# Optimization experiments

Measured on AMD Instinct MI355X. Metric: run time of the kernel, lower is better.

The kernel has to match this reference:

```python
import jax, jax.numpy as jnp
import numpy as np

N, E, G = 20000, 320000, 256
FXD, FXT, OD = 78, 954, 128


def _lin(key, fan_in, fan_out, scale=0.05):
    return jax.random.normal(key, (fan_in, fan_out), dtype=jnp.float32) * scale


def setup_inputs() -> dict:
    key = jax.random.key(0)
    ks = jax.random.split(key, 24)
    inp = {
        "x1": jax.random.normal(ks[0], (N, FXD), dtype=jnp.float32),
        "edge_index1": jax.random.randint(ks[1], (2, E), 0, N, dtype=jnp.int32),
        "batch1": (jnp.arange(N, dtype=jnp.int32) * G) // N,  # sorted, every graph non-empty
        "x2": jax.random.normal(ks[2], (N, FXD), dtype=jnp.float32),
        "edge_index2": jax.random.randint(ks[3], (2, E), 0, N, dtype=jnp.int32),
        "batch2": (jnp.arange(N, dtype=jnp.int32) * G) // N,
        "cell": jax.random.normal(ks[4], (G, FXT), dtype=jnp.float32),
        # GCNConv weights (shared across the two drug branches, as in the module)
        "Wc1": _lin(ks[5], FXD, FXD), "bc1": jnp.zeros((FXD,), jnp.float32),
        "Wc2": _lin(ks[6], FXD, FXD * 2), "bc2": jnp.zeros((FXD * 2,), jnp.float32),
        "Wc3": _lin(ks[7], FXD * 2, FXD * 4), "bc3": jnp.zeros((FXD * 4,), jnp.float32),
        "Wg1": _lin(ks[8], FXD * 4, FXD * 2), "bg1": jnp.zeros((FXD * 2,), jnp.float32),
        "Wg2": _lin(ks[9], FXD * 2, OD), "bg2": jnp.zeros((OD,), jnp.float32),
        # cell reduction MLP 954 -> 2048 -> 512 -> 256
        "Wr1": _lin(ks[10], FXT, 2048), "br1": jnp.zeros((2048,), jnp.float32),
        "Wr2": _lin(ks[11], 2048, 512), "br2": jnp.zeros((512,), jnp.float32),
        "Wr3": _lin(ks[12], 512, OD * 2), "br3": jnp.zeros((OD * 2,), jnp.float32),
        # head MLP 512 -> 1024 -> 512 -> 128 -> 2
        "Wf1": _lin(ks[13], OD * 4, 1024), "bf1": jnp.zeros((1024,), jnp.float32),
        "Wf2": _lin(ks[14], 1024, 512), "bf2": jnp.zeros((512,), jnp.float32),
        "Wf3": _lin(ks[15], 512, 128), "bf3": jnp.zeros((128,), jnp.float32),
        "Wo": _lin(ks[16], 128, 2), "bo": jnp.zeros((2,), jnp.float32),
    }
    return inp


def gcn_conv(x, W, b, src, dst, n):
    """PyG GCNConv: h = D^{-1/2}(A+I)D^{-1/2} (x W) + b (self-loops added)."""
    h = x @ W
    loops = jnp.arange(n, dtype=src.dtype)
    s = jnp.concatenate([src, loops])
    d = jnp.concatenate([dst, loops])
    deg = jax.ops.segment_sum(jnp.ones_like(s, dtype=h.dtype), d, num_segments=n)
    dinv = jax.lax.rsqrt(deg)  # deg >= 1 due to self-loops
    norm = dinv[s] * dinv[d]  # [E+N]
    out = jax.ops.segment_sum(h[s] * norm[:, None], d, num_segments=n)
    return out + b


def drug_branch(x, ei, batch, Wc1, bc1, Wc2, bc2, Wc3, bc3, Wg1, bg1, Wg2, bg2):
    src, dst = ei[0], ei[1]
    n = x.shape[0]
    x = jax.nn.relu(gcn_conv(x, Wc1, bc1, src, dst, n))
    x = jax.nn.relu(gcn_conv(x, Wc2, bc2, src, dst, n))
    x = jax.nn.relu(gcn_conv(x, Wc3, bc3, src, dst, n))
    x = jax.ops.segment_max(x, batch, num_segments=G)  # global max pool -> [G, 312]
    x = jax.nn.relu(x @ Wg1 + bg1)
    x = x @ Wg2 + bg2  # dropout is identity in eval mode
    return x


def reference(x1, edge_index1, batch1, x2, edge_index2, batch2, cell,
              Wc1, bc1, Wc2, bc2, Wc3, bc3, Wg1, bg1, Wg2, bg2,
              Wr1, br1, Wr2, br2, Wr3, br3,
              Wf1, bf1, Wf2, bf2, Wf3, bf3, Wo, bo):
    g1 = drug_branch(x1, edge_index1, batch1, Wc1, bc1, Wc2, bc2, Wc3, bc3, Wg1, bg1, Wg2, bg2)
    g2 = drug_branch(x2, edge_index2, batch2, Wc1, bc1, Wc2, bc2, Wc3, bc3, Wg1, bg1, Wg2, bg2)
    # F.normalize(cell, p=2, dim=1)
    cv = cell / jnp.maximum(jnp.linalg.norm(cell, axis=1, keepdims=True), 1e-12)
    cv = jax.nn.relu(cv @ Wr1 + br1)
    cv = jax.nn.relu(cv @ Wr2 + br2)
    cv = jax.nn.relu(cv @ Wr3 + br3)
    xc = jnp.concatenate([g1, g2, cv], axis=1)  # [G, 512]
    xc = jax.nn.relu(xc @ Wf1 + bf1)
    xc = jax.nn.relu(xc @ Wf2 + bf2)
    xc = jax.nn.relu(xc @ Wf3 + bf3)
    return xc @ Wo + bo  # [G, 2]
```

## Files before the change

### kernel.cpp

```cpp
#include <hip/hip_runtime.h>

#define N_NODES 20000
#define N_EDGES 320000
#define N_GRAPH 256
#define ECHUNK 2048

__device__ __forceinline__ ushort f2b(float f) {
  unsigned u = __float_as_uint(f);
  u += 0x7FFFu + ((u >> 16) & 1u);
  return (ushort)(u >> 16);
}
__device__ __forceinline__ float b2f(ushort u) {
  return __uint_as_float(((unsigned)u) << 16);
}

typedef __attribute__((ext_vector_type(8))) short bf16x8;
typedef __attribute__((ext_vector_type(4))) float f32x4;

template <int POOL>
__launch_bounds__(256)
__global__ void gemm_mfma(const ushort* __restrict__ A, int lda,
                          const ushort* __restrict__ Bt, int ldbt,
                          void* __restrict__ Cv, int ldc, int zstride,
                          const float* __restrict__ bias,
                          int Nr, int Kpad, int M, int do_relu, int obf,
                          int kchunk, int swz,
                          const int* __restrict__ bA, const int* __restrict__ bB,
                          int nsplit, int gA, int gB, int gTot) {
  constexpr int BM = 128, BN = 64, BK = 32, LK = 40;
  __shared__ __align__(16) ushort Asl[BM][LK];
  __shared__ __align__(16) ushort Bsl[BN][LK];
  const int tid = threadIdx.x;
  int bx, by;
  if (swz) {
    const int Cc = (M + BN - 1) / BN;
    const int R = (Nr + BM - 1) / BM;
    const int RR = (R + 7) >> 3;
    const int xz = blockIdx.x & 7, g = blockIdx.x >> 3;
    const int q = g / Cc;
    by = xz * RR + q;
    bx = g - q * Cc;
    if (by >= R) return;
  } else {
    bx = blockIdx.x; by = blockIdx.y;
  }
  const int row0 = by * BM, col0 = bx * BN;

  const int lane = tid & 63, w = tid >> 6;
  const int a_r = tid >> 1, a_h = tid & 1;
  const int b_r = tid >> 2, b_o = (tid & 3) * 8;

  const int klo = blockIdx.z * kchunk;
  const int khi = min(klo + kchunk, Kpad);
  const int nst = (khi - klo) / BK;

  uint4 pa0, pa1, pb0;
  auto load_tile = [&](int k0) {
    if (row0 + a_r < Nr) {
      const uint4* p = (const uint4*)(A + (size_t)(row0 + a_r) * lda + k0 + a_h * 16);
      pa0 = p[0]; pa1 = p[1];
    } else {
      pa0 = make_uint4(0u, 0u, 0u, 0u); pa1 = pa0;
    }
    pb0 = *(const uint4*)(Bt + (size_t)(col0 + b_r) * ldbt + k0 + b_o);
  };
  auto commit = [&]() {
    *(uint4*)&Asl[a_r][a_h * 16] = pa0;
    *(uint4*)&Asl[a_r][a_h * 16 + 8] = pa1;
    *(uint4*)&Bsl[b_r][b_o] = pb0;
  };

  f32x4 acc[2][4] = {};
  const int mrow = w * 32;
  const int lm = lane & 15, lq = (lane >> 4) * 8;

  load_tile(klo);
  for (int t = 0; t < nst; ++t) {
    commit();
    __syncthreads();
    if (t + 1 < nst) load_tile(klo + (t + 1) * BK);
    bf16x8 af0 = *(const bf16x8*)&Asl[mrow + lm][lq];
    bf16x8 af1 = *(const bf16x8*)&Asl[mrow + 16 + lm][lq];
    bf16x8 bf0 = *(const bf16x8*)&Bsl[lm][lq];
    bf16x8 bf1 = *(const bf16x8*)&Bsl[16 + lm][lq];
    bf16x8 bf2 = *(const bf16x8*)&Bsl[32 + lm][lq];
    bf16x8 bf3 = *(const bf16x8*)&Bsl[48 + lm][lq];
    acc[0][0] = __builtin_amdgcn_mfma_f32_16x16x32_bf16(af0, bf0, acc[0][0], 0, 0, 0);
    acc[0][1] = __builtin_amdgcn_mfma_f32_16x16x32_bf16(af0, bf1, acc[0][1], 0, 0, 0);
    acc[0][2] = __builtin_amdgcn_mfma_f32_16x16x32_bf16(af0, bf2, acc[0][2], 0, 0, 0);
    acc[0][3] = __builtin_amdgcn_mfma_f32_16x16x32_bf16(af0, bf3, acc[0][3], 0, 0, 0);
    acc[1][0] = __builtin_amdgcn_mfma_f32_16x16x32_bf16(af1, bf0, acc[1][0], 0, 0, 0);
    acc[1][1] = __builtin_amdgcn_mfma_f32_16x16x32_bf16(af1, bf1, acc[1][1], 0, 0, 0);
    acc[1][2] = __builtin_amdgcn_mfma_f32_16x16x32_bf16(af1, bf2, acc[1][2], 0, 0, 0);
    acc[1][3] = __builtin_amdgcn_mfma_f32_16x16x32_bf16(af1, bf3, acc[1][3], 0, 0, 0);
    __syncthreads();
  }

  const int rquad = (lane >> 4) * 4;

  if constexpr (POOL) {
    __shared__ int Ps[4][64];
    Ps[tid >> 6][tid & 63] = 0;
    __syncthreads();
    const int g0 = (row0 < nsplit) ? gA + bA[row0] : gB + bB[row0 - nsplit];
    int gr8[2][4];
#pragma unroll
    for (int mt = 0; mt < 2; ++mt)
#pragma unroll
      for (int r = 0; r < 4; ++r) {
        const int rr = row0 + mrow + mt * 16 + rquad + r;
        gr8[mt][r] = (rr < Nr)
                         ? ((rr < nsplit) ? gA + bA[rr] : gB + bB[rr - nsplit])
                         : -1;
      }
#pragma unroll
    for (int mt = 0; mt < 2; ++mt)
#pragma unroll
      for (int nt = 0; nt < 4; ++nt) {
        const int cl = nt * 16 + lm;
        if (col0 + cl >= M) continue;
        const float bv = bias[col0 + cl];
#pragma unroll
        for (int r = 0; r < 4; ++r) {
          const int g = gr8[mt][r];
          if (g < 0) continue;
          const float v = fmaxf(acc[mt][nt][r] + bv, 0.f);
          atomicMax(&Ps[g - g0][cl], __float_as_int(v));
        }
      }
    __syncthreads();
    const int s = tid >> 6, c = tid & 63;
    const int g = g0 + s, cc = col0 + c;
    if (g < gTot && cc < M)
      atomicMax((int*)Cv + (size_t)g * ldc + cc, Ps[s][c]);
    return;
  }

  if (zstride) {
    float* Cz = (float*)Cv + (size_t)blockIdx.z * zstride;
#pragma unroll
    for (int mt = 0; mt < 2; ++mt)
#pragma unroll
      for (int nt = 0; nt < 4; ++nt) {
        const int cc = col0 + nt * 16 + lm;
        if (cc >= M) continue;
#pragma unroll
        for (int r = 0; r < 4; ++r) {
          const int rr = row0 + mrow + mt * 16 + rquad + r;
          if (rr < Nr) Cz[(size_t)rr * ldc + cc] = acc[mt][nt][r];
        }
      }
    return;
  }
#pragma unroll
  for (int mt = 0; mt < 2; ++mt) {
#pragma unroll
    for (int nt = 0; nt < 4; ++nt) {
      const int cc = col0 + nt * 16 + lm;
      if (cc >= M) continue;
      const float bv = bias ? bias[cc] : 0.f;
#pragma unroll
      for (int r = 0; r < 4; ++r) {
        const int rr = row0 + mrow + mt * 16 + rquad + r;
        if (rr >= Nr) continue;
        float v = acc[mt][nt][r] + bv;
        if (do_relu) v = fmaxf(v, 0.f);
        if (obf) ((ushort*)Cv)[(size_t)rr * ldc + cc] = f2b(v);
        else     ((float*)Cv)[(size_t)rr * ldc + cc] = v;
      }
    }
  }
}

struct GJob {
  const void* A; const ushort* Bt; void* C; const float* bias;
  int lda, a_f32, ldbt, ldc, Nr, Kpad, M, relu, obf, rsplit, cpad, rb, cb, blk0;
};

__launch_bounds__(256)
__global__ void gemm_grp(GJob j0, GJob j1, int njobs) {
  GJob j = (njobs > 1 && (int)blockIdx.x >= j1.blk0) ? j1 : j0;
  const int local = blockIdx.x - j.blk0;
  const int by = local / j.cb, bx = local - by * j.cb;
  const int row0 = by * 32, col0 = bx * 64;
  const int tid = threadIdx.x, lane = tid & 63, w = tid >> 6;

  __shared__ __align__(16) char smem[32768];
  ushort (*Asl)[32][40] = (ushort (*)[32][40])smem;
  ushort (*Bsl)[64][40] = (ushort (*)[64][40])(smem + 10240);
  float  (*Rs)[32][64]  = (float  (*)[32][64])smem;

  const int a_r = lane >> 1, a_h = lane & 1;
  const int lm = lane & 15, lq = (lane >> 4) * 8;
  const int nst = j.Kpad / 32;

  uint4 ra[4], rb[4];
  auto gload = [&](int t) {
    const int k0 = t * 32;
    const int ar = row0 + a_r;
    if (j.a_f32) {
      if (ar < j.Nr) {
        const uint4* p = (const uint4*)((const float*)j.A + (size_t)ar * j.lda + k0 + a_h * 16);
        ra[0] = p[0]; ra[1] = p[1]; ra[2] = p[2]; ra[3] = p[3];
      } else {
        ra[0] = make_uint4(0u, 0u, 0u, 0u); ra[1] = ra[0]; ra[2] = ra[0]; ra[3] = ra[0];
      }
    } else {
      if (ar < j.Nr) {
        const uint4* p = (const uint4*)((const ushort*)j.A + (size_t)ar * j.lda + k0 + a_h * 16);
        ra[0] = p[0]; ra[1] = p[1];
      } else {
        ra[0] = make_uint4(0u, 0u, 0u, 0u); ra[1] = ra[0];
      }
    }
    const uint4* q = (const uint4*)(j.Bt + (size_t)(col0 + lane) * j.ldbt + k0);
    rb[0] = q[0]; rb[1] = q[1]; rb[2] = q[2]; rb[3] = q[3];
  };
  auto commit = [&]() {
    if (j.a_f32) {
      ushort tmp[16];
      const float* f = (const float*)&ra[0];
#pragma unroll
      for (int q2 = 0; q2 < 16; ++q2) tmp[q2] = f2b(f[q2]);
      *(uint4*)&Asl[w][a_r][a_h * 16]     = *(uint4*)&tmp[0];
      *(uint4*)&Asl[w][a_r][a_h * 16 + 8] = *(uint4*)&tmp[8];
    } else {
      *(uint4*)&Asl[w][a_r][a_h * 16]     = ra[0];
      *(uint4*)&Asl[w][a_r][a_h * 16 + 8] = ra[1];
    }
    *(uint4*)&Bsl[w][lane][0]  = rb[0];
    *(uint4*)&Bsl[w][lane][8]  = rb[1];
    *(uint4*)&Bsl[w][lane][16] = rb[2];
    *(uint4*)&Bsl[w][lane][24] = rb[3];
  };

  f32x4 acc[2][4] = {};
  if (w < nst) {
    gload(w);
    for (int t = w; t < nst; t += 4) {
      commit();
      bf16x8 af0 = *(const bf16x8*)&Asl[w][lm][lq];
      bf16x8 af1 = *(const bf16x8*)&Asl[w][16 + lm][lq];
      bf16x8 bq0 = *(const bf16x8*)&Bsl[w][lm][lq];
      bf16x8 bq1 = *(const bf16x8*)&Bsl[w][16 + lm][lq];
      bf16x8 bq2 = *(const bf16x8*)&Bsl[w][32 + lm][lq];
      bf16x8 bq3 = *(const bf16x8*)&Bsl[w][48 + lm][lq];
      if (t + 4 < nst) gload(t + 4);
      acc[0][0] = __builtin_amdgcn_mfma_f32_16x16x32_bf16(af0, bq0, acc[0][0], 0, 0, 0);
      acc[0][1] = __builtin_amdgcn_mfma_f32_16x16x32_bf16(af0, bq1, acc[0][1], 0, 0, 0);
      acc[0][2] = __builtin_amdgcn_mfma_f32_16x16x32_bf16(af0, bq2, acc[0][2], 0, 0, 0);
      acc[0][3] = __builtin_amdgcn_mfma_f32_16x16x32_bf16(af0, bq3, acc[0][3], 0, 0, 0);
      acc[1][0] = __builtin_amdgcn_mfma_f32_16x16x32_bf16(af1, bq0, acc[1][0], 0, 0, 0);
      acc[1][1] = __builtin_amdgcn_mfma_f32_16x16x32_bf16(af1, bq1, acc[1][1], 0, 0, 0);
      acc[1][2] = __builtin_amdgcn_mfma_f32_16x16x32_bf16(af1, bq2, acc[1][2], 0, 0, 0);
      acc[1][3] = __builtin_amdgcn_mfma_f32_16x16x32_bf16(af1, bq3, acc[1][3], 0, 0, 0);
    }
  }

  __syncthreads();
  const int rquad = (lane >> 4) * 4;
#pragma unroll
  for (int mt = 0; mt < 2; ++mt)
#pragma unroll
    for (int nt = 0; nt < 4; ++nt)
#pragma unroll
      for (int r = 0; r < 4; ++r)
        Rs[w][mt * 16 + rquad + r][nt * 16 + lm] = acc[mt][nt][r];
  __syncthreads();

  const int rrow = tid >> 3, cs = (tid & 7) * 8;
  float v[8];
  {
    float4 x0 = *(const float4*)&Rs[0][rrow][cs];
    float4 x1 = *(const float4*)&Rs[0][rrow][cs + 4];
    v[0] = x0.x; v[1] = x0.y; v[2] = x0.z; v[3] = x0.w;
    v[4] = x1.x; v[5] = x1.y; v[6] = x1.z; v[7] = x1.w;
  }
#pragma unroll
  for (int ww = 1; ww < 4; ++ww) {
    float4 x0 = *(const float4*)&Rs[ww][rrow][cs];
    float4 x1 = *(const float4*)&Rs[ww][rrow][cs + 4];
    v[0] += x0.x; v[1] += x0.y; v[2] += x0.z; v[3] += x0.w;
    v[4] += x1.x; v[5] += x1.y; v[6] += x1.z; v[7] += x1.w;
  }
  const int rg = row0 + rrow;
  if (rg < j.Nr) {
    int rm = rg, rq = 0;
    if (j.rsplit) { rq = rg / j.rsplit; rm = rg - rq * j.rsplit; }
#pragma unroll
    for (int q = 0; q < 8; ++q) {
      const int cc = col0 + cs + q;
      if (cc >= j.cpad) break;
      float x = 0.f;
      if (cc < j.M) {
        x = v[q] + j.bias[cc];
        if (j.relu) x = fmaxf(x, 0.f);
      }
      const size_t di = (size_t)rm * j.ldc + (size_t)rq * j.M + cc;
      if (j.obf) ((ushort*)j.C)[di] = f2b(x);
      else       ((float*)j.C)[di] = x;
    }
  }
}

struct WJob { const float* W; ushort* T; int Mv, Kv, Mp, Kp, blk0; };
struct WArgs { WJob j[11]; int wblocks; const float* cell; ushort* cv; };

__launch_bounds__(256)
__global__ void prep_all(WArgs a) {
  __shared__ float red[256];
  const int bid = blockIdx.x, tid = threadIdx.x;
  if (bid < a.wblocks) {
    int ji = 0;
#pragma unroll
    for (int i = 1; i < 11; ++i)
      if (bid >= a.j[i].blk0) ji = i;
    WJob wj = a.j[ji];
    int el = (bid - wj.blk0) * 256 + tid;
    if (el < wj.Mp * wj.Kp) {
      int n = el / wj.Kp, k = el - n * wj.Kp;
      wj.T[el] = (n < wj.Mv && k < wj.Kv) ? f2b(wj.W[(size_t)k * wj.Mv + n]) : 0;
    }
    return;
  }
  const int g = bid - a.wblocks;
  const float* row = a.cell + (size_t)g * 954;
  float s = 0.f;
  for (int f = tid; f < 954; f += 256) { float vv = row[f]; s += vv * vv; }
  red[tid] = s;
  __syncthreads();
  for (int off2 = 128; off2 > 0; off2 >>= 1) {
    if (tid < off2) red[tid] += red[tid + off2];
    __syncthreads();
  }
  const float inv = 1.f / fmaxf(sqrtf(red[0]), 1e-12f);
  ushort* orow = a.cv + (size_t)g * 960;
  for (int f = tid; f < 954; f += 256) orow[f] = f2b(row[f] * inv);
  for (int f = 954 + tid; f < 960; f += 256) orow[f] = 0;
}

template<int BM, int BN, int TM, int TN>
__launch_bounds__(256)
__global__ void gemm_t(const float* __restrict__ A, int lda,
                       const float* __restrict__ B, int ldb,
                       float* __restrict__ C, int ldc, int zstride,
                       const float* __restrict__ bias,
                       int Nr, int K, int M, int do_relu, int kchunk) {
  constexpr int BK = 16;
  constexpr int LDA = BM + 4;
  __shared__ __align__(16) float As[BK][LDA];
  __shared__ __align__(16) float Bs[BK][BN];
  const int tid = threadIdx.x;
  const int row0 = blockIdx.y * BM, col0 = blockIdx.x * BN;
  constexpr int NX = BN / TN;
  const int tx = tid % NX, ty = tid / NX;
  float acc[TM][TN] = {};
  const int klo = blockIdx.z * kchunk;
  const int khi = min(klo + kchunk, K);

  constexpr int AIT = BM * BK / 4 / 256;
  constexpr int BIT = BK * BN / 4 / 256;
  float4 pa[AIT], pb[BIT];

  auto load_tile = [&](int k0) {
#pragma unroll
    for (int it = 0; it < AIT; ++it) {
      const int s = it * 256 + tid;
      const int row = s >> 2, kq = (s & 3) << 2;
      float4 av = make_float4(0.f, 0.f, 0.f, 0.f);
      const int gr = row0 + row, gk = k0 + kq;
      if (gr < Nr) {
        const float* Ap = A + (size_t)gr * lda + gk;
        if (gk + 3 < khi) { av.x = Ap[0]; av.y = Ap[1]; av.z = Ap[2]; av.w = Ap[3]; }
        else {
          if (gk     < khi) av.x = Ap[0];
          if (gk + 1 < khi) av.y = Ap[1];
          if (gk + 2 < khi) av.z = Ap[2];
        }
      }
      pa[it] = av;
    }
#pragma unroll
    for (int it = 0; it < BIT; ++it) {
      const int s = it * 256 + tid;
      const int kr = s / (BN / 4), c = (s % (BN / 4)) << 2;
      float4 bv = make_float4(0.f, 0.f, 0.f, 0.f);
      const int gk = k0 + kr, gc = col0 + c;
      if (gk < khi) {
        const float* Bp = B + (size_t)gk * ldb + gc;
        if (gc + 3 < M) { bv.x = Bp[0]; bv.y = Bp[1]; bv.z = Bp[2]; bv.w = Bp[3]; }
        else {
          if (gc     < M) bv.x = Bp[0];
          if (gc + 1 < M) bv.y = Bp[1];
          if (gc + 2 < M) bv.z = Bp[2];
        }
      }
      pb[it] = bv;
    }
  };

  load_tile(klo);
  for (int k0 = klo; k0 < khi; k0 += BK) {
#pragma unroll
    for (int it = 0; it < AIT; ++it) {
      const int s = it * 256 + tid;
      const int row = s >> 2, kq = (s & 3) << 2;
      As[kq    ][row] = pa[it].x;
      As[kq + 1][row] = pa[it].y;
      As[kq + 2][row] = pa[it].z;
      As[kq + 3][row] = pa[it].w;
    }
#pragma unroll
    for (int it = 0; it < BIT; ++it) {
      const int s = it * 256 + tid;
      const int kr = s / (BN / 4), c = (s % (BN / 4)) << 2;
      *(float4*)&Bs[kr][c] = pb[it];
    }
    __syncthreads();
    if (k0 + BK < khi) load_tile(k0 + BK);
#pragma unroll
    for (int kk = 0; kk < BK; ++kk) {
      float ar[TM], br[TN];
#pragma unroll
      for (int i = 0; i < TM; i += 4)
        *(float4*)&ar[i] = *(const float4*)&As[kk][ty * TM + i];
      if constexpr (TN == 8) {
        *(float4*)&br[0] = *(const float4*)&Bs[kk][tx * 4];
        *(float4*)&br[4] = *(const float4*)&Bs[kk][BN / 2 + tx * 4];
      } else {
        *(float4*)&br[0] = *(const float4*)&Bs[kk][tx * TN];
      }
#pragma unroll
      for (int i = 0; i < TM; ++i)
#pragma unroll
        for (int j = 0; j < TN; ++j)
          acc[i][j] += ar[i] * br[j];
    }
    __syncthreads();
  }

  float* Cz = C + (size_t)blockIdx.z * zstride;
#pragma unroll
  for (int i = 0; i < TM; ++i) {
    const int r = row0 + ty * TM + i;
    if (r >= Nr) continue;
    float* Crow = Cz + (size_t)r * ldc;
#pragma unroll
    for (int g = 0; g < TN / 4; ++g) {
      const int c = col0 + (TN == 8 ? g * (BN / 2) : 0) + tx * 4;
      if (c + 3 < M) {
        float4 v;
        v.x = acc[i][g * 4 + 0]; v.y = acc[i][g * 4 + 1];
        v.z = acc[i][g * 4 + 2]; v.w = acc[i][g * 4 + 3];
        if (bias) { v.x += bias[c]; v.y += bias[c + 1]; v.z += bias[c + 2]; v.w += bias[c + 3]; }
        if (do_relu) {
          v.x = fmaxf(v.x, 0.f); v.y = fmaxf(v.y, 0.f);
          v.z = fmaxf(v.z, 0.f); v.w = fmaxf(v.w, 0.f);
        }
        *(float4*)&Crow[c] = v;
      } else {
#pragma unroll
        for (int j = 0; j < 4; ++j) {
          if (c + j >= M) continue;
          float v = acc[i][g * 4 + j];
          if (bias) v += bias[c + j];
          if (do_relu) v = fmaxf(v, 0.f);
          Crow[c + j] = v;
        }
      }
    }
  }
}

__global__ void histp_kernel(const int* __restrict__ e1, const int* __restrict__ e2,
                             int* __restrict__ cnt, int E, int npass, int rng) {
  const int xcd = blockIdx.x & 7;
  const int lo = xcd * rng, hi = lo + rng;
  const int base = (blockIdx.x >> 3) * ECHUNK;
  const int TE = npass * E;
  for (int i = threadIdx.x; i < ECHUNK; i += 256) {
    int e = base + i;
    if (e >= TE) break;
    int d = (e < E) ? e1[E + e] : N_NODES + e2[e - E + E];
    if (d >= lo && d < hi) atomicAdd(&cnt[d], 1);
  }
}

__global__ void scat_cvt_kernel(const int* __restrict__ e1, const int* __restrict__ e2,
                                int* __restrict__ cursor, ushort* __restrict__ col_idx,
                                int E, int npass, int rng, int scat_blocks,
                                const float* __restrict__ xa, const float* __restrict__ xb,
                                int nsplit, ushort* __restrict__ dst, int total16) {
  if ((int)blockIdx.x < scat_blocks) {
    const int xcd = blockIdx.x & 7;
    const int lo = xcd * rng, hi = lo + rng;
    const int base = (blockIdx.x >> 3) * ECHUNK;
    const int TE = npass * E;
    for (int i = threadIdx.x; i < ECHUNK; i += 256) {
      int e = base + i;
      if (e >= TE) break;
      int d, s;
      if (e < E) { d = e1[E + e]; s = e1[e]; }
      else { int jj = e - E; d = N_NODES + e2[E + jj]; s = N_NODES + e2[jj]; }
      if (d >= lo && d < hi) {
        int p = atomicAdd(&cursor[d], 1);
        col_idx[p] = (ushort)s;
      }
    }
    return;
  }
  int gid = (blockIdx.x - scat_blocks) * 256 + threadIdx.x;
  if (gid >= total16) return;
  int n = gid / 20, v = gid - n * 20;
  const float* src = (n < nsplit) ? xa + (size_t)n * 78 : xb + (size_t)(n - nsplit) * 78;
  int f0 = v * 4;
  ushort4 o;
  o.x = (f0     < 78) ? f2b(src[f0])     : 0;
  o.y = (f0 + 1 < 78) ? f2b(src[f0 + 1]) : 0;
  o.z = (f0 + 2 < 78) ? f2b(src[f0 + 2]) : 0;
  o.w = (f0 + 3 < 78) ? f2b(src[f0 + 3]) : 0;
  ((ushort4*)(dst + (size_t)n * 80))[v] = o;
}

__launch_bounds__(1024)
__global__ void scan1_kernel(const int* __restrict__ cnt, int* __restrict__ row_ptr,
                             int* __restrict__ part, int n) {
  __shared__ int sh[1024];
  const int tid = threadIdx.x;
  const int i = blockIdx.x * 1024 + tid;
  const int v = (i < n) ? cnt[i] : 0;
  sh[tid] = v;
  __syncthreads();
#pragma unroll
  for (int off = 1; off < 1024; off <<= 1) {
    int t = (tid >= off) ? sh[tid - off] : 0;
    __syncthreads();
    sh[tid] += t;
    __syncthreads();
  }
  if (i < n) row_ptr[i] = sh[tid] - v;
  if (tid == 1023) part[blockIdx.x] = sh[tid];
}

__global__ void scan23_kernel(const int* __restrict__ cnt, int* __restrict__ row_ptr,
                              const int* __restrict__ part, int* __restrict__ cursor,
                              float* __restrict__ dinv, int n, int total,
                              const int* __restrict__ b1, const int* __restrict__ b2,
                              int* __restrict__ s1, int* __restrict__ s2) {
  __shared__ int base_sh;
  const int tid = threadIdx.x;
  if (tid == 0) {
    int blk = blockIdx.x >> 2;
    int s = 0;
    for (int b = 0; b < blk; ++b) s += part[b];
    base_sh = s;
  }
  __syncthreads();
  int i = blockIdx.x * 256 + tid;
  if (i >= n) return;
  int rp = row_ptr[i] + base_sh;
  row_ptr[i] = rp;
  cursor[i] = rp;
  dinv[i] = rsqrtf((float)(cnt[i] + 1));
  if (i == 0) row_ptr[n] = total;
  if (i < N_NODES) {
    if (i == 0) { s1[0] = 0; s1[N_GRAPH] = N_NODES; }
    else if (b1[i] != b1[i - 1]) s1[b1[i]] = i;
  } else {
    int j = i - N_NODES;
    if (j == 0) { s2[0] = N_NODES; s2[N_GRAPH] = 2 * N_NODES; }
    else if (b2[j] != b2[j - 1]) s2[b2[j]] = N_NODES + j;
  }
}

__global__ void aggb_flat(const ushort* __restrict__ h, const int* __restrict__ row_ptr,
                          const ushort* __restrict__ col_idx, const float* __restrict__ dinv,
                          ushort* __restrict__ out, int in_ld, int out_ld,
                          int V, int total) {
  int gid = blockIdx.x * blockDim.x + threadIdx.x;
  if (gid >= total) return;
  int n = gid / V, v = gid - n * V;
  const float din = dinv[n];
  const ushort4* hv = (const ushort4*)h;
  const int ivs = in_ld >> 2;
  float4 a;
  {
    ushort4 u = hv[(size_t)n * ivs + v];
    a.x = din * b2f(u.x); a.y = din * b2f(u.y);
    a.z = din * b2f(u.z); a.w = din * b2f(u.w);
  }
  const int beg = row_ptr[n], end = row_ptr[n + 1];
  int e = beg;
  for (; e + 3 < end; e += 4) {
    int s0 = col_idx[e], s1 = col_idx[e + 1], s2 = col_idx[e + 2], s3 = col_idx[e + 3];
    float d0 = dinv[s0], d1 = dinv[s1], d2 = dinv[s2], d3 = dinv[s3];
    ushort4 u0 = hv[(size_t)s0 * ivs + v], u1 = hv[(size_t)s1 * ivs + v];
    ushort4 u2 = hv[(size_t)s2 * ivs + v], u3 = hv[(size_t)s3 * ivs + v];
    a.x += d0 * b2f(u0.x) + d1 * b2f(u1.x) + d2 * b2f(u2.x) + d3 * b2f(u3.x);
    a.y += d0 * b2f(u0.y) + d1 * b2f(u1.y) + d2 * b2f(u2.y) + d3 * b2f(u3.y);
    a.z += d0 * b2f(u0.z) + d1 * b2f(u1.z) + d2 * b2f(u2.z) + d3 * b2f(u3.z);
    a.w += d0 * b2f(u0.w) + d1 * b2f(u1.w) + d2 * b2f(u2.w) + d3 * b2f(u3.w);
  }
  for (; e < end; ++e) {
    int s0 = col_idx[e];
    float d0 = dinv[s0];
    ushort4 u0 = hv[(size_t)s0 * ivs + v];
    a.x += d0 * b2f(u0.x); a.y += d0 * b2f(u0.y);
    a.z += d0 * b2f(u0.z); a.w += d0 * b2f(u0.w);
  }
  ushort4 o;
  o.x = f2b(din * a.x); o.y = f2b(din * a.y);
  o.z = f2b(din * a.z); o.w = f2b(din * a.w);
  ((ushort4*)(out + (size_t)n * out_ld))[v] = o;
}

extern "C" void kernel_launch(void* const* d_in, const int* in_sizes, int n_in,
                              void* d_out, int out_size, void* d_ws, size_t ws_size,
                              hipStream_t stream) {
  (void)in_sizes; (void)n_in; (void)out_size;
  const float* x1  = (const float*)d_in[0];
  const int*   ei1 = (const int*)d_in[1];
  const int*   bt1 = (const int*)d_in[2];
  const float* x2  = (const float*)d_in[3];
  const int*   ei2 = (const int*)d_in[4];
  const int*   bt2 = (const int*)d_in[5];
  const float* cell = (const float*)d_in[6];
  const float* Wc1 = (const float*)d_in[7];  const float* bc1 = (const float*)d_in[8];
  const float* Wc2 = (const float*)d_in[9];  const float* bc2 = (const float*)d_in[10];
  const float* Wc3 = (const float*)d_in[11]; const float* bc3 = (const float*)d_in[12];
  const float* Wg1 = (const float*)d_in[13]; const float* bg1 = (const float*)d_in[14];
  const float* Wg2 = (const float*)d_in[15]; const float* bg2 = (const float*)d_in[16];
  const float* Wr1 = (const float*)d_in[17]; const float* br1 = (const float*)d_in[18];
  const float* Wr2 = (const float*)d_in[19]; const float* br2 = (const float*)d_in[20];
  const float* Wr3 = (const float*)d_in[21]; const float* br3 = (const float*)d_in[22];
  const float* Wf1 = (const float*)d_in[23]; const float* bf1 = (const float*)d_in[24];
  const float* Wf2 = (const float*)d_in[25]; const float* bf2 = (const float*)d_in[26];
  const float* Wf3 = (const float*)d_in[27]; const float* bf3 = (const float*)d_in[28];
  const float* Wo  = (const float*)d_in[29]; const float* bo  = (const float*)d_in[30];
  float* out = (float*)d_out;

  const bool batched = ws_size >= (size_t)95 * 1024 * 1024;
  const int NPASS = batched ? 2 : 1;
  const int NN = NPASS * N_NODES;

  char* ws = (char*)d_ws;
  size_t off = 0;
  auto alloc_f = [&](size_t ne) {
    ne = (ne + 3) & ~(size_t)3;
    float* p = (float*)(ws + off); off += ne * 4; return p;
  };
  auto alloc_i = [&](size_t ne) {
    ne = (ne + 3) & ~(size_t)3;
    int* p = (int*)(ws + off); off += ne * 4; return p;
  };
  ushort* xb16w = (ushort*)alloc_f((size_t)NN * 80);
  ushort* ab16  = (ushort*)alloc_f((size_t)NN * 80);
  ushort* xb16s = (ushort*)alloc_f((size_t)NN * 40);
  float* dinv   = alloc_f(NN);
  int* cnt      = alloc_i(NN);
  float* pooled = alloc_f((size_t)512 * 320);
  ushort* cv16  = (ushort*)alloc_f((size_t)N_GRAPH * 480);
  ushort* wg1o  = (ushort*)alloc_f((size_t)512 * 80);
  ushort* wr1o  = (ushort*)alloc_f((size_t)256 * 1024);
  ushort* wr2o  = (ushort*)alloc_f((size_t)256 * 256);
  ushort* catbuf = (ushort*)alloc_f((size_t)256 * 256);
  ushort* wf1o  = (ushort*)alloc_f((size_t)256 * 512);
  ushort* wf2o  = (ushort*)alloc_f((size_t)256 * 256);
  float* wf3o   = alloc_f((size_t)256 * 128);
  ushort* wc1t  = (ushort*)alloc_f(128 * 96 / 2);
  ushort* wc2t  = (ushort*)alloc_f(192 * 96 / 2);
  ushort* wc3t  = (ushort*)alloc_f(320 * 160 / 2);
  ushort* wr1t  = (ushort*)alloc_f(2048 * 960 / 2);
  ushort* wr2t  = (ushort*)alloc_f(512 * 2048 / 2);
  ushort* wf1t  = (ushort*)alloc_f(1024 * 512 / 2);
  ushort* wg1t  = (ushort*)alloc_f(192 * 320 / 2);
  ushort* wg2t  = (ushort*)alloc_f(128 * 160 / 2);
  ushort* wr3t  = (ushort*)alloc_f(256 * 512 / 2);
  ushort* wf2t  = (ushort*)alloc_f(512 * 1024 / 2);
  ushort* wf3t  = (ushort*)alloc_f(128 * 512 / 2);
  int* row_ptr = alloc_i(NN + 4);
  int* cursor  = alloc_i(NN);
  ushort* col_idx = (ushort*)alloc_i(NPASS * N_EDGES / 2);
  int* part    = alloc_i(64);
  int* start1  = alloc_i(N_GRAPH + 4);
  int* start2  = alloc_i(N_GRAPH + 4);

  auto gemm_small = [&](const float* A, int lda, const float* B, int ldb, float* C, int ldc,
                        const float* bias, int Nr, int K, int M, int relu) {
    dim3 grid((M + 63) / 64, (Nr + 63) / 64, 1);
    gemm_t<64, 64, 4, 4><<<grid, 256, 0, stream>>>(A, lda, B, ldb, C, ldc, 0, bias,
                                                   Nr, K, M, relu, K);
  };
  auto mfma = [&](const ushort* A, int lda, const ushort* Bt, int ldbt, void* C, int ldc,
                  const float* bias, int Nr, int Kpad, int M, int relu, int obf) {
    int Cc = (M + 63) / 64, R = (Nr + 127) / 128, RR = (R + 7) >> 3;
    dim3 grid(8 * RR * Cc, 1, 1);
    gemm_mfma<0><<<grid, 256, 0, stream>>>(A, lda, Bt, ldbt, C, ldc, 0, bias, Nr, Kpad, M,
                                           relu, obf, Kpad, 1,
                                           nullptr, nullptr, 0, 0, 0, 0);
  };
  auto mfma_pool = [&](const ushort* A, int lda, const ushort* Bt, int ldbt,
                       const float* bias, int Nr, int Kpad, int M,
                       const int* bA, const int* bB, int nsplit, int gA, int gB, int gTot) {
    int Cc = (M + 63) / 64, R = (Nr + 127) / 128, RR = (R + 7) >> 3;
    dim3 grid(8 * RR * Cc, 1, 1);
    gemm_mfma<1><<<grid, 256, 0, stream>>>(A, lda, Bt, ldbt, pooled, 320, 0, bias,
                                           Nr, Kpad, M, 1, 0, Kpad, 1,
                                           bA, bB, nsplit, gA, gB, gTot);
  };
  auto mkjob = [&](const void* A, int lda, int a_f32, const ushort* Bt, int ldbt,
                   void* C, int ldc, const float* bias, int Nr, int Kpad, int M,
                   int relu, int obf, int rsplit, int cpad) {
    GJob g; g.A = A; g.Bt = Bt; g.C = C; g.bias = bias;
    g.lda = lda; g.a_f32 = a_f32; g.ldbt = ldbt; g.ldc = ldc;
    g.Nr = Nr; g.Kpad = Kpad; g.M = M; g.relu = relu; g.obf = obf;
    g.rsplit = rsplit; g.cpad = cpad;
    g.rb = (Nr + 31) / 32; g.cb = (M + 63) / 64; g.blk0 = 0;
    return g;
  };
  auto grp1 = [&](GJob a) {
    gemm_grp<<<a.rb * a.cb, 256, 0, stream>>>(a, a, 1);
  };
  auto grp2 = [&](GJob a, GJob b) {
    b.blk0 = a.rb * a.cb;
    gemm_grp<<<b.blk0 + b.rb * b.cb, 256, 0, stream>>>(a, b, 2);
  };

  {
    WArgs wa{};
    int nj = 0, wb = 0;
    auto addw = [&](const float* W, ushort* T, int Mv, int Kv, int Mp, int Kp) {
      wa.j[nj].W = W; wa.j[nj].T = T; wa.j[nj].Mv = Mv; wa.j[nj].Kv = Kv;
      wa.j[nj].Mp = Mp; wa.j[nj].Kp = Kp; wa.j[nj].blk0 = wb;
      wb += (Mp * Kp + 255) / 256; ++nj;
    };
    addw(Wc1, wc1t,   78,   78,  128,   96);
    addw(Wc2, wc2t,  156,   78,  192,   96);
    addw(Wc3, wc3t,  312,  156,  320,  160);
    addw(Wr1, wr1t, 2048,  954, 2048,  960);
    addw(Wr2, wr2t,  512, 2048,  512, 2048);
    addw(Wf1, wf1t, 1024,  512, 1024,  512);
    addw(Wg1, wg1t,  156,  312,  192,  320);
    addw(Wg2, wg2t,  128,  156,  128,  160);
    addw(Wr3, wr3t,  256,  512,  256,  512);
    addw(Wf2, wf2t,  512, 1024,  512, 1024);
    addw(Wf3, wf3t,  128,  512,  128,  512);
    wa.wblocks = wb; wa.cell = cell; wa.cv = cv16;
    prep_all<<<wb + N_GRAPH, 256, 0, stream>>>(wa);
  }

  auto drug_pass = [&](const float* xa, const float* xb, const int* eia, const int* eib,
                       const int* bta, const int* btb, int npass, int pool_base,
                       int zero_pool) {
    const int nn = npass * N_NODES;
    const int te = npass * N_EDGES;
    const int nb = (nn + 1023) / 1024;
    const int rng = nn / 8;
    const int echunks = (te + ECHUNK - 1) / ECHUNK;
    hipMemsetAsync(cnt, 0, (size_t)nn * 4 + (zero_pool ? (size_t)512 * 320 * 4 : 0),
                   stream);
    histp_kernel<<<8 * echunks, 256, 0, stream>>>(eia, eib, cnt, N_EDGES, npass, rng);
    scan1_kernel<<<nb, 1024, 0, stream>>>(cnt, row_ptr, part, nn);
    scan23_kernel<<<(nn + 255) / 256, 256, 0, stream>>>(cnt, row_ptr, part, cursor, dinv,
                                                        nn, te, bta, btb, start1, start2);
    {
      int nb16 = (nn * 20 + 255) / 256;
      scat_cvt_kernel<<<8 * echunks + nb16, 256, 0, stream>>>(
          eia, eib, cursor, col_idx, N_EDGES, npass, rng, 8 * echunks,
          xa, xb, (npass == 2) ? N_NODES : nn, xb16s, nn * 20);
    }
    {
      int tot = nn * 20;
      aggb_flat<<<(tot + 255) / 256, 256, 0, stream>>>(xb16s, row_ptr, col_idx, dinv,
                                                       ab16, 80, 96, 20, tot);
    }
    mfma(ab16, 96, wc1t, 96, xb16s, 80, bc1, nn, 96, 78, 1, 1);
    {
      int tot = nn * 20;
      aggb_flat<<<(tot + 255) / 256, 256, 0, stream>>>(xb16s, row_ptr, col_idx, dinv,
                                                       ab16, 80, 96, 20, tot);
    }
    mfma(ab16, 96, wc2t, 96, xb16w, 160, bc2, nn, 96, 156, 1, 1);
    {
      int tot = nn * 40;
      aggb_flat<<<(tot + 255) / 256, 256, 0, stream>>>(xb16w, row_ptr, col_idx, dinv,
                                                       ab16, 160, 160, 40, tot);
    }
    mfma_pool(ab16, 160, wc3t, 160, bc3, nn, 160, 312,
              bta, btb, (npass == 2) ? N_NODES : nn,
              pool_base, pool_base + N_GRAPH, pool_base + npass * N_GRAPH);
  };

  if (batched) {
    drug_pass(x1, x2, ei1, ei2, bt1, bt2, 2, 0, 1);
  } else {
    drug_pass(x1, x1, ei1, ei1, bt1, bt1, 1, 0, 1);
    drug_pass(x2, x2, ei2, ei2, bt2, bt2, 1, N_GRAPH, 0);
  }

  grp2(mkjob(pooled, 320, 1, wg1t, 320, wg1o, 160, bg1, 512, 320, 156, 1, 1, 0, 160),
       mkjob(cv16,   960, 0, wr1t, 960, wr1o, 2048, br1, 256, 960, 2048, 1, 1, 0, 2048));
  grp2(mkjob(wg1o,  160, 0, wg2t,  160, catbuf, 512, bg2, 512,  160,  128, 0, 1, 256, 128),
       mkjob(wr1o, 2048, 0, wr2t, 2048, wr2o,   512, br2, 256, 2048,  512, 1, 1, 0, 512));
  grp1(mkjob(wr2o, 512, 0, wr3t, 512, catbuf + 256, 512, br3, 256, 512, 256, 1, 1, 0, 256));
  grp1(mkjob(catbuf, 512, 0, wf1t,  512, wf1o, 1024, bf1, 256,  512, 1024, 1, 1, 0, 1024));
  grp1(mkjob(wf1o,  1024, 0, wf2t, 1024, wf2o,  512, bf2, 256, 1024,  512, 1, 1, 0, 512));
  grp1(mkjob(wf2o,   512, 0, wf3t,  512, wf3o,  128, bf3, 256,  512,  128, 1, 0, 0, 128));
  gemm_small(wf3o, 128, Wo, 2, out, 2, bo, N_GRAPH, 128, 2, 0);
}
```

Before: 430.5 us.

## Pre-scale features by dinv at producer and widen aggregation to 8-wide loads

The source-side D^{-1/2} scaling moves into the producers: the bf16 conversion kernel and the GEMM epilogue now multiply each row by dinv before storing, and they zero the pad columns. This removes the per-edge dinv gather from the SpMM aggregation. The aggregation kernel also switches from ushort4 to uint4 (8 bf16) loads per thread, which halves the thread count and widens the memory transactions. As a trade-off, the pre-scaled values are rounded to bf16 before accumulation, and each thread now carries more registers.

```diff
diff --git a/kernel.cpp b/kernel.cpp
--- a/kernel.cpp
+++ b/kernel.cpp
@@ -25,6 +25,7 @@
                           const float* __restrict__ bias,
                           int Nr, int Kpad, int M, int do_relu, int obf,
                           int kchunk, int swz,
+                          const float* __restrict__ dsc, int cwz,
                           const int* __restrict__ bA, const int* __restrict__ bB,
                           int nsplit, int gA, int gB, int gTot) {
   constexpr int BM = 128, BN = 64, BK = 32, LK = 40;
@@ -152,19 +153,22 @@
       }
     return;
   }
+  const int cz = (cwz > M) ? cwz : M;
 #pragma unroll
   for (int mt = 0; mt < 2; ++mt) {
 #pragma unroll
     for (int nt = 0; nt < 4; ++nt) {
       const int cc = col0 + nt * 16 + lm;
-      if (cc >= M) continue;
-      const float bv = bias ? bias[cc] : 0.f;
+      if (cc >= cz) continue;
+      const bool cval = cc < M;
+      const float bv = (cval && bias) ? bias[cc] : 0.f;
 #pragma unroll
       for (int r = 0; r < 4; ++r) {
         const int rr = row0 + mrow + mt * 16 + rquad + r;
         if (rr >= Nr) continue;
-        float v = acc[mt][nt][r] + bv;
+        float v = cval ? (acc[mt][nt][r] + bv) : 0.f;
         if (do_relu) v = fmaxf(v, 0.f);
+        if (dsc) v *= dsc[rr];
         if (obf) ((ushort*)Cv)[(size_t)rr * ldc + cc] = f2b(v);
         else     ((float*)Cv)[(size_t)rr * ldc + cc] = v;
       }
@@ -490,7 +494,8 @@
                                 int* __restrict__ cursor, ushort* __restrict__ col_idx,
                                 int E, int npass, int rng, int scat_blocks,
                                 const float* __restrict__ xa, const float* __restrict__ xb,
-                                int nsplit, ushort* __restrict__ dst, int total16) {
+                                int nsplit, ushort* __restrict__ dst, int total16,
+                                const float* __restrict__ dinv) {
   if ((int)blockIdx.x < scat_blocks) {
     const int xcd = blockIdx.x & 7;
     const int lo = xcd * rng, hi = lo + rng;
@@ -511,15 +516,15 @@
   }
   int gid = (blockIdx.x - scat_blocks) * 256 + threadIdx.x;
   if (gid >= total16) return;
-  int n = gid / 20, v = gid - n * 20;
+  int n = gid / 10, v = gid - n * 10;
   const float* src = (n < nsplit) ? xa + (size_t)n * 78 : xb + (size_t)(n - nsplit) * 78;
-  int f0 = v * 4;
-  ushort4 o;
-  o.x = (f0     < 78) ? f2b(src[f0])     : 0;
-  o.y = (f0 + 1 < 78) ? f2b(src[f0 + 1]) : 0;
-  o.z = (f0 + 2 < 78) ? f2b(src[f0 + 2]) : 0;
-  o.w = (f0 + 3 < 78) ? f2b(src[f0 + 3]) : 0;
-  ((ushort4*)(dst + (size_t)n * 80))[v] = o;
+  const float sc = dinv[n];
+  const int f0 = v * 8;
+  ushort o[8];
+#pragma unroll
+  for (int jj = 0; jj < 8; ++jj)
+    o[jj] = (f0 + jj < 78) ? f2b(src[f0 + jj] * sc) : 0;
+  ((uint4*)(dst + (size_t)n * 80))[v] = *(uint4*)o;
 }
 
 __launch_bounds__(1024)
@@ -573,6 +578,17 @@
   }
 }
 
+__device__ __forceinline__ void acc8(float* a, uint4 u) {
+  a[0] += __uint_as_float(u.x << 16);
+  a[1] += __uint_as_float(u.x & 0xFFFF0000u);
+  a[2] += __uint_as_float(u.y << 16);
+  a[3] += __uint_as_float(u.y & 0xFFFF0000u);
+  a[4] += __uint_as_float(u.z << 16);
+  a[5] += __uint_as_float(u.z & 0xFFFF0000u);
+  a[6] += __uint_as_float(u.w << 16);
+  a[7] += __uint_as_float(u.w & 0xFFFF0000u);
+}
+
 __global__ void aggb_flat(const ushort* __restrict__ h, const int* __restrict__ row_ptr,
                           const ushort* __restrict__ col_idx, const float* __restrict__ dinv,
                           ushort* __restrict__ out, int in_ld, int out_ld,
@@ -580,38 +596,25 @@
   int gid = blockIdx.x * blockDim.x + threadIdx.x;
   if (gid >= total) return;
   int n = gid / V, v = gid - n * V;
-  const float din = dinv[n];
-  const ushort4* hv = (const ushort4*)h;
-  const int ivs = in_ld >> 2;
-  float4 a;
-  {
-    ushort4 u = hv[(size_t)n * ivs + v];
-    a.x = din * b2f(u.x); a.y = din * b2f(u.y);
-    a.z = din * b2f(u.z); a.w = din * b2f(u.w);
-  }
+  const uint4* hv = (const uint4*)h;
+  const int ivs = in_ld >> 3;
+  float a[8] = {};
+  acc8(a, hv[(size_t)n * ivs + v]);
   const int beg = row_ptr[n], end = row_ptr[n + 1];
   int e = beg;
   for (; e + 3 < end; e += 4) {
     int s0 = col_idx[e], s1 = col_idx[e + 1], s2 = col_idx[e + 2], s3 = col_idx[e + 3];
-    float d0 = dinv[s0], d1 = dinv[s1], d2 = dinv[s2], d3 = dinv[s3];
-    ushort4 u0 = hv[(size_t)s0 * ivs + v], u1 = hv[(size_t)s1 * ivs + v];
-    ushort4 u2 = hv[(size_t)s2 * ivs + v], u3 = hv[(size_t)s3 * ivs + v];
-    a.x += d0 * b2f(u0.x) + d1 * b2f(u1.x) + d2 * b2f(u2.x) + d3 * b2f(u3.x);
-    a.y += d0 * b2f(u0.y) + d1 * b2f(u1.y) + d2 * b2f(u2.y) + d3 * b2f(u3.y);
-    a.z += d0 * b2f(u0.z) + d1 * b2f(u1.z) + d2 * b2f(u2.z) + d3 * b2f(u3.z);
-    a.w += d0 * b2f(u0.w) + d1 * b2f(u1.w) + d2 * b2f(u2.w) + d3 * b2f(u3.w);
-  }
-  for (; e < end; ++e) {
-    int s0 = col_idx[e];
-    float d0 = dinv[s0];
-    ushort4 u0 = hv[(size_t)s0 * ivs + v];
-    a.x += d0 * b2f(u0.x); a.y += d0 * b2f(u0.y);
-    a.z += d0 * b2f(u0.z); a.w += d0 * b2f(u0.w);
-  }
-  ushort4 o;
-  o.x = f2b(din * a.x); o.y = f2b(din * a.y);
-  o.z = f2b(din * a.z); o.w = f2b(din * a.w);
-  ((ushort4*)(out + (size_t)n * out_ld))[v] = o;
+    uint4 u0 = hv[(size_t)s0 * ivs + v], u1 = hv[(size_t)s1 * ivs + v];
+    uint4 u2 = hv[(size_t)s2 * ivs + v], u3 = hv[(size_t)s3 * ivs + v];
+    acc8(a, u0); acc8(a, u1); acc8(a, u2); acc8(a, u3);
+  }
+  for (; e < end; ++e)
+    acc8(a, hv[(size_t)col_idx[e] * ivs + v]);
+  const float din = dinv[n];
+  ushort o[8];
+#pragma unroll
+  for (int jj = 0; jj < 8; ++jj) o[jj] = f2b(din * a[jj]);
+  ((uint4*)(out + (size_t)n * out_ld))[v] = *(uint4*)o;
 }
 
 extern "C" void kernel_launch(void* const* d_in, const int* in_sizes, int n_in,
@@ -692,11 +695,12 @@
                                                    Nr, K, M, relu, K);
   };
   auto mfma = [&](const ushort* A, int lda, const ushort* Bt, int ldbt, void* C, int ldc,
-                  const float* bias, int Nr, int Kpad, int M, int relu, int obf) {
+                  const float* bias, int Nr, int Kpad, int M, int relu, int obf,
+                  const float* dsc, int cwz) {
     int Cc = (M + 63) / 64, R = (Nr + 127) / 128, RR = (R + 7) >> 3;
     dim3 grid(8 * RR * Cc, 1, 1);
     gemm_mfma<0><<<grid, 256, 0, stream>>>(A, lda, Bt, ldbt, C, ldc, 0, bias, Nr, Kpad, M,
-                                           relu, obf, Kpad, 1,
+                                           relu, obf, Kpad, 1, dsc, cwz,
                                            nullptr, nullptr, 0, 0, 0, 0);
   };
   auto mfma_pool = [&](const ushort* A, int lda, const ushort* Bt, int ldbt,
@@ -705,7 +709,7 @@
     int Cc = (M + 63) / 64, R = (Nr + 127) / 128, RR = (R + 7) >> 3;
     dim3 grid(8 * RR * Cc, 1, 1);
     gemm_mfma<1><<<grid, 256, 0, stream>>>(A, lda, Bt, ldbt, pooled, 320, 0, bias,
-                                           Nr, Kpad, M, 1, 0, Kpad, 1,
+                                           Nr, Kpad, M, 1, 0, Kpad, 1, nullptr, 0,
                                            bA, bB, nsplit, gA, gB, gTot);
   };
   auto mkjob = [&](const void* A, int lda, int a_f32, const ushort* Bt, int ldbt,
@@ -764,27 +768,27 @@
     scan23_kernel<<<(nn + 255) / 256, 256, 0, stream>>>(cnt, row_ptr, part, cursor, dinv,
                                                         nn, te, bta, btb, start1, start2);
     {
-      int nb16 = (nn * 20 + 255) / 256;
+      int nb16 = (nn * 10 + 255) / 256;
       scat_cvt_kernel<<<8 * echunks + nb16, 256, 0, stream>>>(
           eia, eib, cursor, col_idx, N_EDGES, npass, rng, 8 * echunks,
-          xa, xb, (npass == 2) ? N_NODES : nn, xb16s, nn * 20);
-    }
+          xa, xb, (npass == 2) ? N_NODES : nn, xb16s, nn * 10, dinv);
+    }
+    {
+      int tot = nn * 10;
+      aggb_flat<<<(tot + 255) / 256, 256, 0, stream>>>(xb16s, row_ptr, col_idx, dinv,
+                                                       ab16, 80, 96, 10, tot);
+    }
+    mfma(ab16, 96, wc1t, 96, xb16s, 80, bc1, nn, 96, 78, 1, 1, dinv, 80);
+    {
+      int tot = nn * 10;
+      aggb_flat<<<(tot + 255) / 256, 256, 0, stream>>>(xb16s, row_ptr, col_idx, dinv,
+                                                       ab16, 80, 96, 10, tot);
+    }
+    mfma(ab16, 96, wc2t, 96, xb16w, 160, bc2, nn, 96, 156, 1, 1, dinv, 160);
     {
       int tot = nn * 20;
-      aggb_flat<<<(tot + 255) / 256, 256, 0, stream>>>(xb16s, row_ptr, col_idx, dinv,
-                                                       ab16, 80, 96, 20, tot);
-    }
-    mfma(ab16, 96, wc1t, 96, xb16s, 80, bc1, nn, 96, 78, 1, 1);
-    {
-      int tot = nn * 20;
-      aggb_flat<<<(tot + 255) / 256, 256, 0, stream>>>(xb16s, row_ptr, col_idx, dinv,
-                                                       ab16, 80, 96, 20, tot);
-    }
-    mfma(ab16, 96, wc2t, 96, xb16w, 160, bc2, nn, 96, 156, 1, 1);
-    {
-      int tot = nn * 40;
       aggb_flat<<<(tot + 255) / 256, 256, 0, stream>>>(xb16w, row_ptr, col_idx, dinv,
-                                                       ab16, 160, 160, 40, tot);
+                                                       ab16, 160, 160, 20, tot);
     }
     mfma_pool(ab16, 160, wc3t, 160, bc3, nn, 160, 312,
               bta, btb, (npass == 2) ? N_NODES : nn,
```

Result: no change. 424.5 us (-1.4%).
